# Kernel optimization log

Measured on AMD Instinct MI355X. Metric: run time of the kernel, lower is better.

The kernel has to match this reference:

```python
import jax, jax.numpy as jnp
import numpy as np

B, S, H = 4, 2048, 1024
EXP_BITS, SIG_BITS = 5, 10  # rmode=1 -> round-to-nearest


def quantize(x):
    """Simulated low-precision float quantization (LightChop-style) with STE.

    exp_bits exponent bits (bias = 2^(e-1)-1, exponent clamped -> subnormal
    handling falls out of the clamp), sig_bits significand bits, round-to-nearest.
    """
    bias = 2 ** (EXP_BITS - 1) - 1
    ax = jnp.abs(x)
    e = jnp.floor(jnp.log2(jnp.where(ax > 0, ax, 1.0)))
    e = jnp.clip(e, 1 - bias, bias)               # clamp to representable exponent range
    scale = jnp.exp2(e - SIG_BITS)                # ulp at this exponent
    q = jnp.round(x / scale) * scale              # round significand to SIG_BITS bits
    max_val = (2.0 - 2.0 ** (-SIG_BITS)) * 2.0 ** bias
    q = jnp.clip(q, -max_val, max_val)            # saturate overflow
    # straight-through estimator: forward = q, backward = identity
    return x + jax.lax.stop_gradient(q - x)


def setup_inputs() -> dict:
    key = jax.random.key(0)
    ks = jax.random.split(key, 7)
    w_scale = 1.0 / np.sqrt(H)
    return {
        "x": jax.random.normal(ks[0], (B, S, H), dtype=jnp.float32),
        "Wq": jax.random.normal(ks[1], (H, H), dtype=jnp.float32) * w_scale,
        "bq": jax.random.normal(ks[2], (H,), dtype=jnp.float32) * 0.01,
        "Wk": jax.random.normal(ks[3], (H, H), dtype=jnp.float32) * w_scale,
        "bk": jax.random.normal(ks[4], (H,), dtype=jnp.float32) * 0.01,
        "Wv": jax.random.normal(ks[5], (H, H), dtype=jnp.float32) * w_scale,
        "bv": jax.random.normal(ks[6], (H,), dtype=jnp.float32) * 0.01,
    }


def reference(x, Wq, bq, Wk, bk, Wv, bv):
    # nn.Linear: y = x @ W.T + b   (W stored [out, in])
    q = quantize(jnp.einsum("bsh,oh->bso", x, Wq) + bq)
    k = quantize(jnp.einsum("bsh,oh->bso", x, Wk) + bk)
    v = quantize(jnp.einsum("bsh,oh->bso", x, Wv) + bv)
    inv_sqrt_h = 1.0 / (H ** 0.5)
    scores = quantize(jnp.einsum("bsh,bth->bst", q, k) * inv_sqrt_h)  # [B,S,S]
    attn = quantize(jax.nn.softmax(scores, axis=-1))
    return jnp.einsum("bst,bth->bsh", attn, v)
```

## Files before the change

### kernel.cpp

```cpp
#include <hip/hip_runtime.h>
#include <hip/hip_fp16.h>

#define B_ 4
#define S_ 2048
#define H_ 1024
#define M_ (B_ * S_)

typedef _Float16 f16;
typedef _Float16 f16x8 __attribute__((ext_vector_type(8)));
typedef _Float16 f16x4 __attribute__((ext_vector_type(4)));
typedef float f32x4 __attribute__((ext_vector_type(4)));

typedef __attribute__((address_space(3))) unsigned int* lds_u32p;
typedef const __attribute__((address_space(1))) unsigned int* gbl_u32p;

__device__ __forceinline__ void stage16(const f16* g, f16* l) {
  __builtin_amdgcn_global_load_lds((gbl_u32p)g, (lds_u32p)l, 16, 0, 0);
}

__global__ __launch_bounds__(256) void downconvert_x(const float* __restrict__ x,
                                                     f16* __restrict__ hi, int n4) {
  int i = blockIdx.x * 256 + threadIdx.x;
  if (i >= n4) return;
  f32x4 v = ((const f32x4*)x)[i];
  f16x4 h;
#pragma unroll
  for (int c = 0; c < 4; c++) h[c] = (f16)v[c];
  ((f16x4*)hi)[i] = h;
}

__global__ __launch_bounds__(256) void downconvert_w(const float* __restrict__ W0,
                                                     const float* __restrict__ W1,
                                                     const float* __restrict__ W2,
                                                     f16* __restrict__ hi) {
  const int sel = blockIdx.y;
  const float* W = sel == 0 ? W0 : (sel == 1 ? W1 : W2);
  int i = blockIdx.x * 256 + threadIdx.x;
  f32x4 v = ((const f32x4*)W)[i];
  f16x4 h;
#pragma unroll
  for (int c = 0; c < 4; c++) h[c] = (f16)v[c];
  ((f16x4*)(hi + (long)sel * H_ * H_))[i] = h;
}

__global__ __launch_bounds__(256, 2)
void qkv_gemm(const f16* __restrict__ xh, const f16* __restrict__ Wh,
              const float* __restrict__ bq, const float* __restrict__ bk,
              const float* __restrict__ bv, f16* __restrict__ qkv) {
  __shared__ __align__(16) f16 As[128 * 32];
  __shared__ __align__(16) f16 Bs[128 * 32];
  const int t = threadIdx.x;
  const int wave = t >> 6, lane = t & 63;
  const int quad = lane >> 4, l16 = lane & 15;
  const int wm = (wave & 1) * 64, wn = (wave >> 1) * 64;
  const int sel = blockIdx.y >> 3;
  const int ntile = (blockIdx.y & 7) * 128;
  const int mtile = blockIdx.x * 128;

  const f16* Ab = xh + (long)mtile * H_;
  const f16* Bb = Wh + (long)sel * H_ * H_ + (long)ntile * H_;

  const int r0 = t >> 2;
  const int c8 = (t & 3) * 8;

  f32x4 acc[4][4] = {};

  for (int k0 = 0; k0 < H_; k0 += 32) {
    __syncthreads();
    stage16(Ab + (long)r0 * H_ + k0 + c8,        As + t * 8);
    stage16(Ab + (long)(r0 + 64) * H_ + k0 + c8, As + 2048 + t * 8);
    stage16(Bb + (long)r0 * H_ + k0 + c8,        Bs + t * 8);
    stage16(Bb + (long)(r0 + 64) * H_ + k0 + c8, Bs + 2048 + t * 8);
    __syncthreads();
    f16x8 ah[4], bh[4];
#pragma unroll
    for (int i = 0; i < 4; i++) {
      ah[i] = *(const f16x8*)&As[(wm + i * 16 + l16) * 32 + quad * 8];
      bh[i] = *(const f16x8*)&Bs[(wn + i * 16 + l16) * 32 + quad * 8];
    }
#pragma unroll
    for (int i = 0; i < 4; i++)
#pragma unroll
      for (int j = 0; j < 4; j++)
        acc[i][j] = __builtin_amdgcn_mfma_f32_16x16x32_f16(ah[i], bh[j], acc[i][j], 0, 0, 0);
  }

  const float* bias = sel == 0 ? bq : (sel == 1 ? bk : bv);
  f16* out = qkv + (long)sel * M_ * H_;
#pragma unroll
  for (int j = 0; j < 4; j++) {
    int n = ntile + wn + j * 16 + l16;
    float bb = bias[n];
#pragma unroll
    for (int i = 0; i < 4; i++) {
      int m = mtile + wm + i * 16 + quad * 4;
#pragma unroll
      for (int r = 0; r < 4; r++)
        out[(long)(m + r) * H_ + n] = (f16)(acc[i][j][r] + bb);
    }
  }
}

template <int OUT_F16>
__global__ __launch_bounds__(256, 2)
void gemm_nt(const f16* __restrict__ A, const f16* __restrict__ Bm,
             void* __restrict__ C, int lda, int ldb, int ldc, int K,
             long sA, long sB, long sC, float alpha) {
  __shared__ __align__(16) f16 As[128 * 32];
  __shared__ __align__(16) f16 Bs[128 * 32];
  const int t = threadIdx.x;
  const int wave = t >> 6, lane = t & 63;
  const int quad = lane >> 4, l16 = lane & 15;
  const int wm = (wave & 1) * 64, wn = (wave >> 1) * 64;
  const f16* Ab = A + blockIdx.z * sA + (long)blockIdx.x * 128 * lda;
  const f16* Bb = Bm + blockIdx.z * sB + (long)blockIdx.y * 128 * ldb;
  const int r0 = t >> 2, c8 = (t & 3) * 8;
  f32x4 acc[4][4] = {};
  for (int k0 = 0; k0 < K; k0 += 32) {
    __syncthreads();
    stage16(Ab + (long)r0 * lda + k0 + c8,        As + t * 8);
    stage16(Ab + (long)(r0 + 64) * lda + k0 + c8, As + 2048 + t * 8);
    stage16(Bb + (long)r0 * ldb + k0 + c8,        Bs + t * 8);
    stage16(Bb + (long)(r0 + 64) * ldb + k0 + c8, Bs + 2048 + t * 8);
    __syncthreads();
    f16x8 af[4], bf[4];
#pragma unroll
    for (int i = 0; i < 4; i++) {
      af[i] = *(const f16x8*)&As[(wm + i * 16 + l16) * 32 + quad * 8];
      bf[i] = *(const f16x8*)&Bs[(wn + i * 16 + l16) * 32 + quad * 8];
    }
#pragma unroll
    for (int i = 0; i < 4; i++)
#pragma unroll
      for (int j = 0; j < 4; j++)
        acc[i][j] = __builtin_amdgcn_mfma_f32_16x16x32_f16(af[i], bf[j], acc[i][j], 0, 0, 0);
  }
  const long mb = (long)blockIdx.x * 128 + wm;
  const long nb = (long)blockIdx.y * 128 + wn;
#pragma unroll
  for (int i = 0; i < 4; i++)
#pragma unroll
    for (int j = 0; j < 4; j++) {
      long m = mb + i * 16 + quad * 4;
      long n = nb + j * 16 + l16;
#pragma unroll
      for (int r = 0; r < 4; r++) {
        float v = acc[i][j][r] * alpha;
        if (OUT_F16)
          ((f16*)C)[blockIdx.z * sC + (m + r) * ldc + n] = (f16)v;
        else
          ((float*)C)[blockIdx.z * sC + (m + r) * ldc + n] = v;
      }
    }
}

__global__ __launch_bounds__(256) void transpose_v(const f16* __restrict__ v,
                                                   f16* __restrict__ vT) {
  __shared__ __align__(16) f16 tile[64][72];
  const int b = blockIdx.z;
  const int t0 = blockIdx.x * 64;
  const int h0 = blockIdx.y * 64;
  const int t = threadIdx.x;
  const int tx = t & 7, ty = t >> 3;
#pragma unroll
  for (int it = 0; it < 2; it++) {
    int r = ty + it * 32;
    f16x8 vv = *(const f16x8*)&v[((long)(b * S_ + t0 + r)) * H_ + h0 + tx * 8];
#pragma unroll
    for (int c = 0; c < 8; c++) tile[tx * 8 + c][r] = vv[c];
  }
  __syncthreads();
#pragma unroll
  for (int it = 0; it < 2; it++) {
    int r = ty + it * 32;
    f16x8 vv = *(const f16x8*)&tile[r][tx * 8];
    *(f16x8*)&vT[((long)(b * H_ + h0 + r)) * S_ + t0 + tx * 8] = vv;
  }
}

__global__ __launch_bounds__(256) void softmax_q(f16* __restrict__ sc) {
  const long row = blockIdx.x;
  f16* p = sc + row * S_;
  const int t = threadIdx.x;
  const int wave = t >> 6, lane = t & 63;
  f16x8 v = ((const f16x8*)p)[t];
  float f[8];
  float m = -3.0e38f;
#pragma unroll
  for (int c = 0; c < 8; c++) { f[c] = (float)v[c]; m = fmaxf(m, f[c]); }
#pragma unroll
  for (int o = 32; o > 0; o >>= 1) m = fmaxf(m, __shfl_xor(m, o));
  __shared__ float redm[4], reds[4];
  if (lane == 0) redm[wave] = m;
  __syncthreads();
  m = fmaxf(fmaxf(redm[0], redm[1]), fmaxf(redm[2], redm[3]));
  float s = 0.f, e[8];
#pragma unroll
  for (int c = 0; c < 8; c++) { e[c] = __expf(f[c] - m); s += e[c]; }
#pragma unroll
  for (int o = 32; o > 0; o >>= 1) s += __shfl_xor(s, o);
  if (lane == 0) reds[wave] = s;
  __syncthreads();
  s = reds[0] + reds[1] + reds[2] + reds[3];
  float inv = 1.0f / s;
  f16x8 ov;
#pragma unroll
  for (int c = 0; c < 8; c++) ov[c] = (f16)(e[c] * inv);
  ((f16x8*)p)[t] = ov;
}

extern "C" void kernel_launch(void* const* d_in, const int* in_sizes, int n_in,
                              void* d_out, int out_size, void* d_ws, size_t ws_size,
                              hipStream_t stream) {
  (void)in_sizes; (void)n_in; (void)out_size; (void)ws_size;
  const float* x  = (const float*)d_in[0];
  const float* Wq = (const float*)d_in[1];
  const float* bq = (const float*)d_in[2];
  const float* Wk = (const float*)d_in[3];
  const float* bk = (const float*)d_in[4];
  const float* Wv = (const float*)d_in[5];
  const float* bv = (const float*)d_in[6];

  char* ws = (char*)d_ws;
  f16* xh  = (f16*)ws; ws += (size_t)M_ * H_ * 2;
  f16* Wh  = (f16*)ws; ws += (size_t)3 * H_ * H_ * 2;
  f16* qkv = (f16*)ws; ws += (size_t)3 * M_ * H_ * 2;
  f16* vT  = (f16*)ws; ws += (size_t)B_ * H_ * S_ * 2;
  f16* sc  = (f16*)ws; ws += (size_t)B_ * S_ * S_ * 2;

  downconvert_x<<<M_ * H_ / 4 / 256, 256, 0, stream>>>(x, xh, M_ * H_ / 4);
  downconvert_w<<<dim3(H_ * H_ / 4 / 256, 3), 256, 0, stream>>>(Wq, Wk, Wv, Wh);

  qkv_gemm<<<dim3(64, 24), 256, 0, stream>>>(xh, Wh, bq, bk, bv, qkv);

  transpose_v<<<dim3(32, 16, 4), 256, 0, stream>>>(qkv + (size_t)2 * M_ * H_, vT);

  gemm_nt<1><<<dim3(16, 16, 4), 256, 0, stream>>>(
      qkv, qkv + (size_t)M_ * H_, sc, H_, H_, S_, H_,
      (long)S_ * H_, (long)S_ * H_, (long)S_ * S_, 0.03125f);

  softmax_q<<<M_, 256, 0, stream>>>(sc);

  gemm_nt<0><<<dim3(16, 8, 4), 256, 0, stream>>>(
      sc, vT, d_out, S_, S_, H_, S_,
      (long)S_ * S_, (long)H_ * S_, (long)S_ * H_, 1.0f);
}
```

Before: 284.9 us.

## Fuse V transpose into QKV epilogue, merge downconverts, widen K step to 64

The two fp32-to-fp16 conversion kernels are merged into a single launch. The QKV GEMM epilogue now writes V directly in transposed layout with packed 4-element stores, which removes the separate transpose kernel and its extra read and write of V. Both GEMMs stage 64 K-columns per barrier pair instead of 32, halving the number of synchronisations, at the cost of doubling shared-memory use per block, which could limit occupancy.

```diff
diff --git a/kernel.cpp b/kernel.cpp
--- a/kernel.cpp
+++ b/kernel.cpp
@@ -18,37 +18,38 @@
   __builtin_amdgcn_global_load_lds((gbl_u32p)g, (lds_u32p)l, 16, 0, 0);
 }
 
-__global__ __launch_bounds__(256) void downconvert_x(const float* __restrict__ x,
-                                                     f16* __restrict__ hi, int n4) {
-  int i = blockIdx.x * 256 + threadIdx.x;
-  if (i >= n4) return;
-  f32x4 v = ((const f32x4*)x)[i];
+__global__ __launch_bounds__(256) void downconvert_all(
+    const float* __restrict__ x, const float* __restrict__ W0,
+    const float* __restrict__ W1, const float* __restrict__ W2,
+    f16* __restrict__ xh, f16* __restrict__ Wh) {
+  const int b = blockIdx.x;
+  const float* src;
+  f16* dst;
+  long i;
+  if (b < M_ * H_ / 1024) {
+    src = x; dst = xh;
+    i = (long)b * 256 + threadIdx.x;
+  } else {
+    const int wb = b - M_ * H_ / 1024;
+    const int sel = wb >> 10;
+    src = sel == 0 ? W0 : (sel == 1 ? W1 : W2);
+    dst = Wh + (long)sel * H_ * H_;
+    i = (long)(wb & 1023) * 256 + threadIdx.x;
+  }
+  f32x4 v = ((const f32x4*)src)[i];
   f16x4 h;
 #pragma unroll
   for (int c = 0; c < 4; c++) h[c] = (f16)v[c];
-  ((f16x4*)hi)[i] = h;
-}
-
-__global__ __launch_bounds__(256) void downconvert_w(const float* __restrict__ W0,
-                                                     const float* __restrict__ W1,
-                                                     const float* __restrict__ W2,
-                                                     f16* __restrict__ hi) {
-  const int sel = blockIdx.y;
-  const float* W = sel == 0 ? W0 : (sel == 1 ? W1 : W2);
-  int i = blockIdx.x * 256 + threadIdx.x;
-  f32x4 v = ((const f32x4*)W)[i];
-  f16x4 h;
-#pragma unroll
-  for (int c = 0; c < 4; c++) h[c] = (f16)v[c];
-  ((f16x4*)(hi + (long)sel * H_ * H_))[i] = h;
+  ((f16x4*)dst)[i] = h;
 }
 
 __global__ __launch_bounds__(256, 2)
 void qkv_gemm(const f16* __restrict__ xh, const f16* __restrict__ Wh,
               const float* __restrict__ bq, const float* __restrict__ bk,
-              const float* __restrict__ bv, f16* __restrict__ qkv) {
-  __shared__ __align__(16) f16 As[128 * 32];
-  __shared__ __align__(16) f16 Bs[128 * 32];
+              const float* __restrict__ bv, f16* __restrict__ qkv,
+              f16* __restrict__ vT) {
+  __shared__ __align__(16) f16 As[2 * 128 * 32];
+  __shared__ __align__(16) f16 Bs[2 * 128 * 32];
   const int t = threadIdx.x;
   const int wave = t >> 6, lane = t & 63;
   const int quad = lane >> 4, l16 = lane & 15;
@@ -65,38 +66,61 @@
 
   f32x4 acc[4][4] = {};
 
-  for (int k0 = 0; k0 < H_; k0 += 32) {
-    __syncthreads();
-    stage16(Ab + (long)r0 * H_ + k0 + c8,        As + t * 8);
-    stage16(Ab + (long)(r0 + 64) * H_ + k0 + c8, As + 2048 + t * 8);
-    stage16(Bb + (long)r0 * H_ + k0 + c8,        Bs + t * 8);
-    stage16(Bb + (long)(r0 + 64) * H_ + k0 + c8, Bs + 2048 + t * 8);
-    __syncthreads();
-    f16x8 ah[4], bh[4];
-#pragma unroll
-    for (int i = 0; i < 4; i++) {
-      ah[i] = *(const f16x8*)&As[(wm + i * 16 + l16) * 32 + quad * 8];
-      bh[i] = *(const f16x8*)&Bs[(wn + i * 16 + l16) * 32 + quad * 8];
-    }
-#pragma unroll
-    for (int i = 0; i < 4; i++)
-#pragma unroll
-      for (int j = 0; j < 4; j++)
-        acc[i][j] = __builtin_amdgcn_mfma_f32_16x16x32_f16(ah[i], bh[j], acc[i][j], 0, 0, 0);
+  for (int k0 = 0; k0 < H_; k0 += 64) {
+    __syncthreads();
+    stage16(Ab + (long)r0 * H_ + k0 + c8,             As + t * 8);
+    stage16(Ab + (long)(r0 + 64) * H_ + k0 + c8,      As + 2048 + t * 8);
+    stage16(Ab + (long)r0 * H_ + k0 + 32 + c8,        As + 4096 + t * 8);
+    stage16(Ab + (long)(r0 + 64) * H_ + k0 + 32 + c8, As + 6144 + t * 8);
+    stage16(Bb + (long)r0 * H_ + k0 + c8,             Bs + t * 8);
+    stage16(Bb + (long)(r0 + 64) * H_ + k0 + c8,      Bs + 2048 + t * 8);
+    stage16(Bb + (long)r0 * H_ + k0 + 32 + c8,        Bs + 4096 + t * 8);
+    stage16(Bb + (long)(r0 + 64) * H_ + k0 + 32 + c8, Bs + 6144 + t * 8);
+    __syncthreads();
+#pragma unroll
+    for (int kk = 0; kk < 2; kk++) {
+      f16x8 ah[4], bh[4];
+#pragma unroll
+      for (int i = 0; i < 4; i++) {
+        ah[i] = *(const f16x8*)&As[kk * 4096 + (wm + i * 16 + l16) * 32 + quad * 8];
+        bh[i] = *(const f16x8*)&Bs[kk * 4096 + (wn + i * 16 + l16) * 32 + quad * 8];
+      }
+#pragma unroll
+      for (int i = 0; i < 4; i++)
+#pragma unroll
+        for (int j = 0; j < 4; j++)
+          acc[i][j] = __builtin_amdgcn_mfma_f32_16x16x32_f16(ah[i], bh[j], acc[i][j], 0, 0, 0);
+    }
   }
 
   const float* bias = sel == 0 ? bq : (sel == 1 ? bk : bv);
-  f16* out = qkv + (long)sel * M_ * H_;
-#pragma unroll
-  for (int j = 0; j < 4; j++) {
-    int n = ntile + wn + j * 16 + l16;
-    float bb = bias[n];
-#pragma unroll
-    for (int i = 0; i < 4; i++) {
-      int m = mtile + wm + i * 16 + quad * 4;
-#pragma unroll
-      for (int r = 0; r < 4; r++)
-        out[(long)(m + r) * H_ + n] = (f16)(acc[i][j][r] + bb);
+  if (sel == 2) {
+#pragma unroll
+    for (int j = 0; j < 4; j++) {
+      int n = ntile + wn + j * 16 + l16;
+      float bb = bias[n];
+#pragma unroll
+      for (int i = 0; i < 4; i++) {
+        int m = mtile + wm + i * 16 + quad * 4;
+        f16x4 pack;
+#pragma unroll
+        for (int r = 0; r < 4; r++) pack[r] = (f16)(acc[i][j][r] + bb);
+        *(f16x4*)&vT[((long)(m >> 11) * H_ + n) * S_ + (m & 2047)] = pack;
+      }
+    }
+  } else {
+    f16* out = qkv + (long)sel * M_ * H_;
+#pragma unroll
+    for (int j = 0; j < 4; j++) {
+      int n = ntile + wn + j * 16 + l16;
+      float bb = bias[n];
+#pragma unroll
+      for (int i = 0; i < 4; i++) {
+        int m = mtile + wm + i * 16 + quad * 4;
+#pragma unroll
+        for (int r = 0; r < 4; r++)
+          out[(long)(m + r) * H_ + n] = (f16)(acc[i][j][r] + bb);
+      }
     }
   }
 }
@@ -106,8 +130,8 @@
 void gemm_nt(const f16* __restrict__ A, const f16* __restrict__ Bm,
              void* __restrict__ C, int lda, int ldb, int ldc, int K,
              long sA, long sB, long sC, float alpha) {
-  __shared__ __align__(16) f16 As[128 * 32];
-  __shared__ __align__(16) f16 Bs[128 * 32];
+  __shared__ __align__(16) f16 As[2 * 128 * 32];
+  __shared__ __align__(16) f16 Bs[2 * 128 * 32];
   const int t = threadIdx.x;
   const int wave = t >> 6, lane = t & 63;
   const int quad = lane >> 4, l16 = lane & 15;
@@ -116,24 +140,31 @@
   const f16* Bb = Bm + blockIdx.z * sB + (long)blockIdx.y * 128 * ldb;
   const int r0 = t >> 2, c8 = (t & 3) * 8;
   f32x4 acc[4][4] = {};
-  for (int k0 = 0; k0 < K; k0 += 32) {
-    __syncthreads();
-    stage16(Ab + (long)r0 * lda + k0 + c8,        As + t * 8);
-    stage16(Ab + (long)(r0 + 64) * lda + k0 + c8, As + 2048 + t * 8);
-    stage16(Bb + (long)r0 * ldb + k0 + c8,        Bs + t * 8);
-    stage16(Bb + (long)(r0 + 64) * ldb + k0 + c8, Bs + 2048 + t * 8);
-    __syncthreads();
-    f16x8 af[4], bf[4];
-#pragma unroll
-    for (int i = 0; i < 4; i++) {
-      af[i] = *(const f16x8*)&As[(wm + i * 16 + l16) * 32 + quad * 8];
-      bf[i] = *(const f16x8*)&Bs[(wn + i * 16 + l16) * 32 + quad * 8];
-    }
-#pragma unroll
-    for (int i = 0; i < 4; i++)
-#pragma unroll
-      for (int j = 0; j < 4; j++)
-        acc[i][j] = __builtin_amdgcn_mfma_f32_16x16x32_f16(af[i], bf[j], acc[i][j], 0, 0, 0);
+  for (int k0 = 0; k0 < K; k0 += 64) {
+    __syncthreads();
+    stage16(Ab + (long)r0 * lda + k0 + c8,             As + t * 8);
+    stage16(Ab + (long)(r0 + 64) * lda + k0 + c8,      As + 2048 + t * 8);
+    stage16(Ab + (long)r0 * lda + k0 + 32 + c8,        As + 4096 + t * 8);
+    stage16(Ab + (long)(r0 + 64) * lda + k0 + 32 + c8, As + 6144 + t * 8);
+    stage16(Bb + (long)r0 * ldb + k0 + c8,             Bs + t * 8);
+    stage16(Bb + (long)(r0 + 64) * ldb + k0 + c8,      Bs + 2048 + t * 8);
+    stage16(Bb + (long)r0 * ldb + k0 + 32 + c8,        Bs + 4096 + t * 8);
+    stage16(Bb + (long)(r0 + 64) * ldb + k0 + 32 + c8, Bs + 6144 + t * 8);
+    __syncthreads();
+#pragma unroll
+    for (int kk = 0; kk < 2; kk++) {
+      f16x8 af[4], bf[4];
+#pragma unroll
+      for (int i = 0; i < 4; i++) {
+        af[i] = *(const f16x8*)&As[kk * 4096 + (wm + i * 16 + l16) * 32 + quad * 8];
+        bf[i] = *(const f16x8*)&Bs[kk * 4096 + (wn + i * 16 + l16) * 32 + quad * 8];
+      }
+#pragma unroll
+      for (int i = 0; i < 4; i++)
+#pragma unroll
+        for (int j = 0; j < 4; j++)
+          acc[i][j] = __builtin_amdgcn_mfma_f32_16x16x32_f16(af[i], bf[j], acc[i][j], 0, 0, 0);
+    }
   }
   const long mb = (long)blockIdx.x * 128 + wm;
   const long nb = (long)blockIdx.y * 128 + wn;
@@ -152,30 +183,6 @@
           ((float*)C)[blockIdx.z * sC + (m + r) * ldc + n] = v;
       }
     }
-}
-
-__global__ __launch_bounds__(256) void transpose_v(const f16* __restrict__ v,
-                                                   f16* __restrict__ vT) {
-  __shared__ __align__(16) f16 tile[64][72];
-  const int b = blockIdx.z;
-  const int t0 = blockIdx.x * 64;
-  const int h0 = blockIdx.y * 64;
-  const int t = threadIdx.x;
-  const int tx = t & 7, ty = t >> 3;
-#pragma unroll
-  for (int it = 0; it < 2; it++) {
-    int r = ty + it * 32;
-    f16x8 vv = *(const f16x8*)&v[((long)(b * S_ + t0 + r)) * H_ + h0 + tx * 8];
-#pragma unroll
-    for (int c = 0; c < 8; c++) tile[tx * 8 + c][r] = vv[c];
-  }
-  __syncthreads();
-#pragma unroll
-  for (int it = 0; it < 2; it++) {
-    int r = ty + it * 32;
-    f16x8 vv = *(const f16x8*)&tile[r][tx * 8];
-    *(f16x8*)&vT[((long)(b * H_ + h0 + r)) * S_ + t0 + tx * 8] = vv;
-  }
 }
 
 __global__ __launch_bounds__(256) void softmax_q(f16* __restrict__ sc) {
@@ -224,16 +231,14 @@
   char* ws = (char*)d_ws;
   f16* xh  = (f16*)ws; ws += (size_t)M_ * H_ * 2;
   f16* Wh  = (f16*)ws; ws += (size_t)3 * H_ * H_ * 2;
-  f16* qkv = (f16*)ws; ws += (size_t)3 * M_ * H_ * 2;
+  f16* qkv = (f16*)ws; ws += (size_t)2 * M_ * H_ * 2;
   f16* vT  = (f16*)ws; ws += (size_t)B_ * H_ * S_ * 2;
   f16* sc  = (f16*)ws; ws += (size_t)B_ * S_ * S_ * 2;
 
-  downconvert_x<<<M_ * H_ / 4 / 256, 256, 0, stream>>>(x, xh, M_ * H_ / 4);
-  downconvert_w<<<dim3(H_ * H_ / 4 / 256, 3), 256, 0, stream>>>(Wq, Wk, Wv, Wh);
-
-  qkv_gemm<<<dim3(64, 24), 256, 0, stream>>>(xh, Wh, bq, bk, bv, qkv);
-
-  transpose_v<<<dim3(32, 16, 4), 256, 0, stream>>>(qkv + (size_t)2 * M_ * H_, vT);
+  downconvert_all<<<M_ * H_ / 1024 + 3 * H_ * H_ / 1024, 256, 0, stream>>>(
+      x, Wq, Wk, Wv, xh, Wh);
+
+  qkv_gemm<<<dim3(64, 24), 256, 0, stream>>>(xh, Wh, bq, bk, bv, qkv, vT);
 
   gemm_nt<1><<<dim3(16, 16, 4), 256, 0, stream>>>(
       qkv, qkv + (size_t)M_ * H_, sc, H_, H_, S_, H_,
```

Result: faster. 252.0 us (-11.5%).
